# Kernel tuning notes

Hardware: AMD Instinct MI355X
Metric: run time of the kernel (lower is better)

The kernel has to match this reference:

```python
import jax, jax.numpy as jnp
import numpy as np

BATCH, SEQ_LEN, D_MODEL, STATE_DIM = 8, 4096, 512, 64
LN_EPS = 1e-5


def _hippo_log_neg_eigs(state_dim):
    A = np.zeros((state_dim, state_dim))
    for i in range(state_dim):
        for j in range(state_dim):
            if i > j:
                A[i, j] = -((2 * i + 1) ** 0.5) * ((2 * j + 1) ** 0.5)
            elif i == j:
                A[i, j] = -(i + 1)
    ev = np.sort(np.linalg.eigvals(A).real)[:state_dim]
    return np.log(-ev + 1e-06).astype(np.float32)


def setup_inputs() -> dict:
    key = jax.random.key(0)
    ks = jax.random.split(key, 8)
    d, s = D_MODEL, STATE_DIM
    return {
        "x": jax.random.normal(ks[0], (BATCH, SEQ_LEN, d), dtype=jnp.float32),
        "log_A": jnp.asarray(_hippo_log_neg_eigs(s)),
        "B": jax.random.normal(ks[1], (d, s), dtype=jnp.float32) * 0.01,
        "C": jax.random.normal(ks[2], (s, d), dtype=jnp.float32) * 0.01,
        "D": jnp.zeros((d,), dtype=jnp.float32),
        "log_dt": jnp.zeros((), dtype=jnp.float32),
        "gamma": jnp.ones((d,), dtype=jnp.float32),
        "beta": jnp.zeros((d,), dtype=jnp.float32),
        "W1": jax.random.normal(ks[3], (d, 2 * d), dtype=jnp.float32) * (1.0 / np.sqrt(d)),
        "b1": jnp.zeros((2 * d,), dtype=jnp.float32),
        "W2": jax.random.normal(ks[4], (2 * d, d), dtype=jnp.float32) * (1.0 / np.sqrt(2 * d)),
        "b2": jnp.zeros((d,), dtype=jnp.float32),
    }


def _layernorm(x, gamma, beta):
    mu = jnp.mean(x, axis=-1, keepdims=True)
    var = jnp.mean(jnp.square(x - mu), axis=-1, keepdims=True)
    return (x - mu) * jax.lax.rsqrt(var + LN_EPS) * gamma + beta


def reference(x, log_A, B, C, D, log_dt, gamma, beta, W1, b1, W2, b2):
    residual = x
    xn = _layernorm(x, gamma, beta)  # [B, L, D]

    dt = jnp.exp(log_dt)
    A_bar = jnp.exp(-jnp.exp(log_A) * dt)  # [S]

    # Precompute input projections for all timesteps, then scan the diagonal recurrence.
    xB = jnp.einsum("bld,ds->lbs", xn, B)  # [L, B, S]
    h0 = jnp.zeros((xn.shape[0], A_bar.shape[0]), dtype=xn.dtype)

    def step(h, xb_t):
        h = A_bar * h + xb_t
        return h, h

    _, hs = jax.lax.scan(step, h0, xB)  # hs: [L, B, S]

    y = jnp.einsum("lbs,sd->bld", hs, C) + xn * D  # [B, L, D]
    y = y + residual

    yn = _layernorm(y, gamma, beta)
    mlp = jax.nn.gelu(yn @ W1 + b1, approximate=False) @ W2 + b2
    return y + mlp
```

## Files before the change

### kernel.cpp

```cpp
#include <hip/hip_runtime.h>
#include <math.h>

#define BATCH 8
#define SEQL 4096
#define DMODEL 512
#define SDIM 64
#define MROWS (BATCH * SEQL)
#define LN_EPS 1e-5f

typedef __attribute__((ext_vector_type(8))) short bf16x8;
typedef __attribute__((ext_vector_type(4))) float f32x4;

__device__ __forceinline__ float wave_sum(float v) {
#pragma unroll
  for (int off = 32; off > 0; off >>= 1) v += __shfl_xor(v, off, 64);
  return v;
}

__device__ __forceinline__ unsigned short f2bf(float f) {
  unsigned int u = __float_as_uint(f);
  u += 0x7fffu + ((u >> 16) & 1u);
  return (unsigned short)(u >> 16);
}

__device__ __forceinline__ float gelu_exact(float v) {
  return 0.5f * v * (1.0f + erff(v * 0.70710678118654752f));
}

__device__ __forceinline__ void gl2lds16(const void* g, void* l) {
  __builtin_amdgcn_global_load_lds((const __attribute__((address_space(1))) void*)g,
                                   (__attribute__((address_space(3))) void*)l, 16, 0, 0);
}

__global__ void ln_stats_kernel(const float* __restrict__ x, float* __restrict__ mu,
                                float* __restrict__ rstd) {
  int row = blockIdx.x * 4 + (threadIdx.x >> 6);
  int lane = threadIdx.x & 63;
  const float4* xp = (const float4*)(x + (size_t)row * DMODEL);
  float4 a = xp[lane * 2];
  float4 b = xp[lane * 2 + 1];
  float s = a.x + a.y + a.z + a.w + b.x + b.y + b.z + b.w;
  float q = a.x * a.x + a.y * a.y + a.z * a.z + a.w * a.w + b.x * b.x + b.y * b.y +
            b.z * b.z + b.w * b.w;
  s = wave_sum(s);
  q = wave_sum(q);
  if (lane == 0) {
    float m = s * (1.0f / DMODEL);
    float var = q * (1.0f / DMODEL) - m * m;
    mu[row] = m;
    rstd[row] = rsqrtf(var + LN_EPS);
  }
}

__global__ __launch_bounds__(256) void xb_gemm_kernel(
    const float* __restrict__ x, const float* __restrict__ mu, const float* __restrict__ rstd,
    const float* __restrict__ gamma, const float* __restrict__ beta,
    const float* __restrict__ Bm, float* __restrict__ xB) {
  __shared__ float aT[32 * 68];
  __shared__ float bT[32 * 64];
  const int t = threadIdx.x;
  const int m0 = blockIdx.x * 64;
  const int ty = t >> 4, tx = t & 15;
  const int r0 = ty * 4, c0 = tx * 4;
  const int lrow = t >> 2, lseg = t & 3;
  const int bk = t >> 3, bseg = t & 7;
  const float mr = mu[m0 + lrow];
  const float rr = rstd[m0 + lrow];
  float acc[4][4] = {};
  for (int k0 = 0; k0 < DMODEL; k0 += 32) {
    __syncthreads();
    {
      const float* xp = x + (size_t)(m0 + lrow) * DMODEL + k0 + lseg * 8;
      float4 v0 = *(const float4*)xp;
      float4 v1 = *(const float4*)(xp + 4);
      float4 g0 = *(const float4*)(gamma + k0 + lseg * 8);
      float4 g1 = *(const float4*)(gamma + k0 + lseg * 8 + 4);
      float4 e0 = *(const float4*)(beta + k0 + lseg * 8);
      float4 e1 = *(const float4*)(beta + k0 + lseg * 8 + 4);
      const int kb = lseg * 8;
      aT[(kb + 0) * 68 + lrow] = (v0.x - mr) * rr * g0.x + e0.x;
      aT[(kb + 1) * 68 + lrow] = (v0.y - mr) * rr * g0.y + e0.y;
      aT[(kb + 2) * 68 + lrow] = (v0.z - mr) * rr * g0.z + e0.z;
      aT[(kb + 3) * 68 + lrow] = (v0.w - mr) * rr * g0.w + e0.w;
      aT[(kb + 4) * 68 + lrow] = (v1.x - mr) * rr * g1.x + e1.x;
      aT[(kb + 5) * 68 + lrow] = (v1.y - mr) * rr * g1.y + e1.y;
      aT[(kb + 6) * 68 + lrow] = (v1.z - mr) * rr * g1.z + e1.z;
      aT[(kb + 7) * 68 + lrow] = (v1.w - mr) * rr * g1.w + e1.w;
      const float* bp = Bm + (size_t)(k0 + bk) * SDIM + bseg * 8;
      *(float4*)&bT[bk * 64 + bseg * 8] = *(const float4*)bp;
      *(float4*)&bT[bk * 64 + bseg * 8 + 4] = *(const float4*)(bp + 4);
    }
    __syncthreads();
#pragma unroll
    for (int kk = 0; kk < 32; ++kk) {
      float4 av = *(const float4*)&aT[kk * 68 + r0];
      float4 bv = *(const float4*)&bT[kk * 64 + c0];
      float ar[4] = {av.x, av.y, av.z, av.w};
      float br[4] = {bv.x, bv.y, bv.z, bv.w};
#pragma unroll
      for (int i = 0; i < 4; ++i)
#pragma unroll
        for (int j = 0; j < 4; ++j) acc[i][j] += ar[i] * br[j];
    }
  }
#pragma unroll
  for (int i = 0; i < 4; ++i) {
    *(float4*)&xB[(size_t)(m0 + r0 + i) * SDIM + c0] =
        make_float4(acc[i][0], acc[i][1], acc[i][2], acc[i][3]);
  }
}

__global__ void scan_ends_kernel(const float* __restrict__ xB, const float* __restrict__ logA,
                                 const float* __restrict__ logdt, float* __restrict__ ends) {
  int t = blockIdx.x * 256 + threadIdx.x;
  int s = t & 63;
  int c = (t >> 6) & 63;
  int b = t >> 12;
  float a = expf(-expf(logA[s]) * expf(logdt[0]));
  const float* p = xB + ((size_t)(b * SEQL + c * 64)) * SDIM + s;
  float e = 0.0f;
#pragma unroll
  for (int i = 0; i < 64; ++i) e = a * e + p[(size_t)i * SDIM];
  ends[(b * 64 + c) * 64 + s] = e;
}

__global__ void scan_carry_kernel(const float* __restrict__ ends, const float* __restrict__ logA,
                                  const float* __restrict__ logdt,
                                  float* __restrict__ carries) {
  int t = blockIdx.x * 256 + threadIdx.x;
  int s = t & 63;
  int b = t >> 6;
  float a = expf(-expf(logA[s]) * expf(logdt[0]));
  float a64 = a;
#pragma unroll
  for (int i = 0; i < 6; ++i) a64 *= a64;
  float carry = 0.0f;
  for (int c = 0; c < 64; ++c) {
    carries[(b * 64 + c) * 64 + s] = carry;
    carry = a64 * carry + ends[(b * 64 + c) * 64 + s];
  }
}

__global__ void scan_fix_kernel(const float* __restrict__ logA, const float* __restrict__ logdt,
                                const float* __restrict__ carries, float* __restrict__ xB) {
  int t = blockIdx.x * 256 + threadIdx.x;
  int s = t & 63;
  int c = (t >> 6) & 63;
  int b = t >> 12;
  float a = expf(-expf(logA[s]) * expf(logdt[0]));
  float h = carries[(b * 64 + c) * 64 + s];
  float* p = xB + ((size_t)(b * SEQL + c * 64)) * SDIM + s;
#pragma unroll
  for (int i = 0; i < 64; ++i) {
    h = a * h + p[(size_t)i * SDIM];
    p[(size_t)i * SDIM] = h;
  }
}

__global__ __launch_bounds__(256) void y_gemm_kernel(
    const float* __restrict__ hs, const float* __restrict__ Cm, const float* __restrict__ x,
    const float* __restrict__ mu, const float* __restrict__ rstd,
    const float* __restrict__ gamma, const float* __restrict__ beta,
    const float* __restrict__ Dv, float* __restrict__ out) {
  __shared__ float aT[64 * 68];
  __shared__ float bT[64 * 64];
  const int t = threadIdx.x;
  const int m0 = blockIdx.y * 64;
  const int n0 = blockIdx.x * 64;
  const int ty = t >> 4, tx = t & 15;
  const int r0 = ty * 4, c0 = tx * 4;
  const int lrow = t >> 2, lseg = t & 3;
  {
    const float* hp = hs + (size_t)(m0 + lrow) * SDIM + lseg * 16;
#pragma unroll
    for (int u = 0; u < 4; ++u) {
      float4 v = *(const float4*)(hp + u * 4);
      int kb = lseg * 16 + u * 4;
      aT[(kb + 0) * 68 + lrow] = v.x;
      aT[(kb + 1) * 68 + lrow] = v.y;
      aT[(kb + 2) * 68 + lrow] = v.z;
      aT[(kb + 3) * 68 + lrow] = v.w;
    }
    const float* cp = Cm + (size_t)lrow * DMODEL + n0 + lseg * 16;
#pragma unroll
    for (int u = 0; u < 4; ++u)
      *(float4*)&bT[lrow * 64 + lseg * 16 + u * 4] = *(const float4*)(cp + u * 4);
  }
  __syncthreads();
  float acc[4][4] = {};
#pragma unroll 16
  for (int kk = 0; kk < 64; ++kk) {
    float4 av = *(const float4*)&aT[kk * 68 + r0];
    float4 bv = *(const float4*)&bT[kk * 64 + c0];
    float ar[4] = {av.x, av.y, av.z, av.w};
    float br[4] = {bv.x, bv.y, bv.z, bv.w};
#pragma unroll
    for (int i = 0; i < 4; ++i)
#pragma unroll
      for (int j = 0; j < 4; ++j) acc[i][j] += ar[i] * br[j];
  }
  const int cg = n0 + c0;
  float4 gv = *(const float4*)&gamma[cg];
  float4 ev = *(const float4*)&beta[cg];
  float4 dv = *(const float4*)&Dv[cg];
#pragma unroll
  for (int i = 0; i < 4; ++i) {
    int m = m0 + r0 + i;
    float4 xv = *(const float4*)&x[(size_t)m * DMODEL + cg];
    float mm = mu[m], rr = rstd[m];
    float o0 = acc[i][0] + ((xv.x - mm) * rr * gv.x + ev.x) * dv.x + xv.x;
    float o1 = acc[i][1] + ((xv.y - mm) * rr * gv.y + ev.y) * dv.y + xv.y;
    float o2 = acc[i][2] + ((xv.z - mm) * rr * gv.z + ev.z) * dv.z + xv.z;
    float o3 = acc[i][3] + ((xv.w - mm) * rr * gv.w + ev.w) * dv.w + xv.w;
    *(float4*)&out[(size_t)m * DMODEL + cg] = make_float4(o0, o1, o2, o3);
  }
}

__global__ void ln_apply_kernel(const float* __restrict__ y, const float* __restrict__ gamma,
                                const float* __restrict__ beta,
                                unsigned short* __restrict__ yn) {
  int row = blockIdx.x * 4 + (threadIdx.x >> 6);
  int lane = threadIdx.x & 63;
  const float4* yp = (const float4*)(y + (size_t)row * DMODEL);
  float4 a = yp[lane * 2];
  float4 b = yp[lane * 2 + 1];
  float s = a.x + a.y + a.z + a.w + b.x + b.y + b.z + b.w;
  float q = a.x * a.x + a.y * a.y + a.z * a.z + a.w * a.w + b.x * b.x + b.y * b.y +
            b.z * b.z + b.w * b.w;
  s = wave_sum(s);
  q = wave_sum(q);
  float m = s * (1.0f / DMODEL);
  float var = q * (1.0f / DMODEL) - m * m;
  float rs = rsqrtf(var + LN_EPS);
  const float4* gp = (const float4*)gamma;
  const float4* bp = (const float4*)beta;
  float4 g0 = gp[lane * 2], g1 = gp[lane * 2 + 1];
  float4 e0 = bp[lane * 2], e1 = bp[lane * 2 + 1];
  float o0x = (a.x - m) * rs * g0.x + e0.x, o0y = (a.y - m) * rs * g0.y + e0.y;
  float o0z = (a.z - m) * rs * g0.z + e0.z, o0w = (a.w - m) * rs * g0.w + e0.w;
  float o1x = (b.x - m) * rs * g1.x + e1.x, o1y = (b.y - m) * rs * g1.y + e1.y;
  float o1z = (b.z - m) * rs * g1.z + e1.z, o1w = (b.w - m) * rs * g1.w + e1.w;
  uint4 pk;
  pk.x = (unsigned)f2bf(o0x) | ((unsigned)f2bf(o0y) << 16);
  pk.y = (unsigned)f2bf(o0z) | ((unsigned)f2bf(o0w) << 16);
  pk.z = (unsigned)f2bf(o1x) | ((unsigned)f2bf(o1y) << 16);
  pk.w = (unsigned)f2bf(o1z) | ((unsigned)f2bf(o1w) << 16);
  ((uint4*)(yn + (size_t)row * DMODEL))[lane] = pk;
}

__global__ __launch_bounds__(256) void transpose_bf16_kernel(const float* __restrict__ W,
                                                             unsigned short* __restrict__ Wt,
                                                             int K, int N) {
  __shared__ unsigned short tile[64][65];
  int k0 = blockIdx.y * 64, n0 = blockIdx.x * 64;
  int tx = threadIdx.x & 15, ty = threadIdx.x >> 4;
#pragma unroll
  for (int p = 0; p < 4; ++p) {
    int k = p * 16 + ty;
    float4 v = *(const float4*)&W[(size_t)(k0 + k) * N + n0 + tx * 4];
    tile[tx * 4 + 0][k] = f2bf(v.x);
    tile[tx * 4 + 1][k] = f2bf(v.y);
    tile[tx * 4 + 2][k] = f2bf(v.z);
    tile[tx * 4 + 3][k] = f2bf(v.w);
  }
  __syncthreads();
#pragma unroll
  for (int p = 0; p < 4; ++p) {
    int n = p * 16 + ty;
    ushort4 o;
    o.x = tile[n][tx * 4 + 0];
    o.y = tile[n][tx * 4 + 1];
    o.z = tile[n][tx * 4 + 2];
    o.w = tile[n][tx * 4 + 3];
    *(ushort4*)&Wt[(size_t)(n0 + n) * K + k0 + tx * 4] = o;
  }
}

__global__ __launch_bounds__(256) void mlp1_mfma_kernel(const unsigned short* __restrict__ yn,
                                                        const unsigned short* __restrict__ w1t,
                                                        const float* __restrict__ b1,
                                                        unsigned short* __restrict__ g) {
  __shared__ unsigned short As[128 * 32];
  __shared__ unsigned short Bs[128 * 32];
  const int t = threadIdx.x;
  const int wave = t >> 6, lane = t & 63;
  const int m0 = blockIdx.y * 128, n0 = blockIdx.x * 128;
  const int wm = (wave >> 1) * 64, wn = (wave & 1) * 64;
  const int row0 = t >> 2, seg0 = t & 3;
  const int row1 = (t + 256) >> 2, seg1 = t & 3;
  const unsigned short* gA0 = yn + (size_t)(m0 + row0) * 512 + seg0 * 8;
  const unsigned short* gA1 = yn + (size_t)(m0 + row1) * 512 + seg1 * 8;
  const unsigned short* gB0 = w1t + (size_t)(n0 + row0) * 512 + seg0 * 8;
  const unsigned short* gB1 = w1t + (size_t)(n0 + row1) * 512 + seg1 * 8;
  unsigned short* lA0 = As + (size_t)(wave * 64) * 8;
  unsigned short* lA1 = As + (size_t)(256 + wave * 64) * 8;
  unsigned short* lB0 = Bs + (size_t)(wave * 64) * 8;
  unsigned short* lB1 = Bs + (size_t)(256 + wave * 64) * 8;
  f32x4 acc[4][4] = {};
  const int fr = lane & 15, fq = lane >> 4;
  for (int k0 = 0; k0 < 512; k0 += 32) {
    __syncthreads();
    gl2lds16(gA0 + k0, lA0);
    gl2lds16(gA1 + k0, lA1);
    gl2lds16(gB0 + k0, lB0);
    gl2lds16(gB1 + k0, lB1);
    __syncthreads();
#pragma unroll
    for (int i = 0; i < 4; ++i) {
      bf16x8 a = *(const bf16x8*)&As[(wm + i * 16 + fr) * 32 + fq * 8];
#pragma unroll
      for (int j = 0; j < 4; ++j) {
        bf16x8 b = *(const bf16x8*)&Bs[(wn + j * 16 + fr) * 32 + fq * 8];
        acc[i][j] = __builtin_amdgcn_mfma_f32_16x16x32_bf16(a, b, acc[i][j], 0, 0, 0);
      }
    }
  }
#pragma unroll
  for (int i = 0; i < 4; ++i)
#pragma unroll
    for (int j = 0; j < 4; ++j) {
      const int cg = n0 + wn + j * 16 + fr;
      const float bb = b1[cg];
#pragma unroll
      for (int r = 0; r < 4; ++r) {
        const int rg = m0 + wm + i * 16 + fq * 4 + r;
        g[(size_t)rg * 1024 + cg] = f2bf(gelu_exact(acc[i][j][r] + bb));
      }
    }
}

__global__ __launch_bounds__(256) void mlp2_mfma_kernel(const unsigned short* __restrict__ g,
                                                        const unsigned short* __restrict__ w2t,
                                                        const float* __restrict__ b2,
                                                        float* __restrict__ out) {
  __shared__ unsigned short As[128 * 32];
  __shared__ unsigned short Bs[128 * 32];
  const int t = threadIdx.x;
  const int wave = t >> 6, lane = t & 63;
  const int m0 = blockIdx.y * 128, n0 = blockIdx.x * 128;
  const int wm = (wave >> 1) * 64, wn = (wave & 1) * 64;
  const int row0 = t >> 2, seg0 = t & 3;
  const int row1 = (t + 256) >> 2, seg1 = t & 3;
  const unsigned short* gA0 = g + (size_t)(m0 + row0) * 1024 + seg0 * 8;
  const unsigned short* gA1 = g + (size_t)(m0 + row1) * 1024 + seg1 * 8;
  const unsigned short* gB0 = w2t + (size_t)(n0 + row0) * 1024 + seg0 * 8;
  const unsigned short* gB1 = w2t + (size_t)(n0 + row1) * 1024 + seg1 * 8;
  unsigned short* lA0 = As + (size_t)(wave * 64) * 8;
  unsigned short* lA1 = As + (size_t)(256 + wave * 64) * 8;
  unsigned short* lB0 = Bs + (size_t)(wave * 64) * 8;
  unsigned short* lB1 = Bs + (size_t)(256 + wave * 64) * 8;
  f32x4 acc[4][4] = {};
  const int fr = lane & 15, fq = lane >> 4;
  for (int k0 = 0; k0 < 1024; k0 += 32) {
    __syncthreads();
    gl2lds16(gA0 + k0, lA0);
    gl2lds16(gA1 + k0, lA1);
    gl2lds16(gB0 + k0, lB0);
    gl2lds16(gB1 + k0, lB1);
    __syncthreads();
#pragma unroll
    for (int i = 0; i < 4; ++i) {
      bf16x8 a = *(const bf16x8*)&As[(wm + i * 16 + fr) * 32 + fq * 8];
#pragma unroll
      for (int j = 0; j < 4; ++j) {
        bf16x8 b = *(const bf16x8*)&Bs[(wn + j * 16 + fr) * 32 + fq * 8];
        acc[i][j] = __builtin_amdgcn_mfma_f32_16x16x32_bf16(a, b, acc[i][j], 0, 0, 0);
      }
    }
  }
#pragma unroll
  for (int i = 0; i < 4; ++i)
#pragma unroll
    for (int j = 0; j < 4; ++j) {
      const int cg = n0 + wn + j * 16 + fr;
      const float bb = b2[cg];
#pragma unroll
      for (int r = 0; r < 4; ++r) {
        const int rg = m0 + wm + i * 16 + fq * 4 + r;
        const size_t off = (size_t)rg * 512 + cg;
        out[off] = out[off] + acc[i][j][r] + bb;
      }
    }
}

extern "C" void kernel_launch(void* const* d_in, const int* in_sizes, int n_in, void* d_out,
                              int out_size, void* d_ws, size_t ws_size, hipStream_t stream) {
  const float* x = (const float*)d_in[0];
  const float* logA = (const float*)d_in[1];
  const float* Bm = (const float*)d_in[2];
  const float* Cm = (const float*)d_in[3];
  const float* Dv = (const float*)d_in[4];
  const float* logdt = (const float*)d_in[5];
  const float* gamma = (const float*)d_in[6];
  const float* beta = (const float*)d_in[7];
  const float* W1 = (const float*)d_in[8];
  const float* b1 = (const float*)d_in[9];
  const float* W2 = (const float*)d_in[10];
  const float* b2 = (const float*)d_in[11];
  float* out = (float*)d_out;

  char* ws = (char*)d_ws;
  float* mu1 = (float*)(ws + 0);
  float* rstd1 = (float*)(ws + 131072);
  float* ends = (float*)(ws + 262144);
  float* carries = (float*)(ws + 393216);
  float* xB = (float*)(ws + 524288);
  unsigned short* yn = (unsigned short*)(ws + 8912896);
  unsigned short* g = (unsigned short*)(ws + 42467328);
  unsigned short* w1t = (unsigned short*)(ws + 109576192);
  unsigned short* w2t = (unsigned short*)(ws + 110624768);

  transpose_bf16_kernel<<<dim3(1024 / 64, 512 / 64), 256, 0, stream>>>(W1, w1t, 512, 1024);
  transpose_bf16_kernel<<<dim3(512 / 64, 1024 / 64), 256, 0, stream>>>(W2, w2t, 1024, 512);

  ln_stats_kernel<<<MROWS / 4, 256, 0, stream>>>(x, mu1, rstd1);
  xb_gemm_kernel<<<MROWS / 64, 256, 0, stream>>>(x, mu1, rstd1, gamma, beta, Bm, xB);
  scan_ends_kernel<<<128, 256, 0, stream>>>(xB, logA, logdt, ends);
  scan_carry_kernel<<<2, 256, 0, stream>>>(ends, logA, logdt, carries);
  scan_fix_kernel<<<128, 256, 0, stream>>>(logA, logdt, carries, xB);
  y_gemm_kernel<<<dim3(DMODEL / 64, MROWS / 64), 256, 0, stream>>>(xB, Cm, x, mu1, rstd1, gamma,
                                                                   beta, Dv, out);
  ln_apply_kernel<<<MROWS / 4, 256, 0, stream>>>(out, gamma, beta, yn);
  mlp1_mfma_kernel<<<dim3(1024 / 128, MROWS / 128), 256, 0, stream>>>(yn, w1t, b1, g);
  mlp2_mfma_kernel<<<dim3(512 / 128, MROWS / 128), 256, 0, stream>>>(g, w2t, b2, out);
}
```

Baseline: 368.9 us.

## Move SSM projections to bf16 MFMA, fuse y GEMM with second layernorm

The input projection x·B now runs on bf16 MFMA. LayerNorm is folded algebraically: gamma is pre-multiplied into B, and the mean and beta terms are applied in the epilogue from precomputed sums, with x converted to bf16 during the stats pass. The scan writes hidden states as bf16, and one fused kernel computes the C projection with MFMA, the residual, and the second layernorm, producing both out and the bf16 normalized activations. Exact erf GELU is replaced by a polynomial approximation. This removes the fp32 FMA GEMMs and one full pass over the activations, at the cost of extra bf16 rounding and larger LDS use in the fused kernel.

```diff
diff --git a/kernel.cpp b/kernel.cpp
--- a/kernel.cpp
+++ b/kernel.cpp
@@ -23,8 +23,16 @@
   return (unsigned short)(u >> 16);
 }
 
-__device__ __forceinline__ float gelu_exact(float v) {
-  return 0.5f * v * (1.0f + erff(v * 0.70710678118654752f));
+__device__ __forceinline__ float gelu_fast(float v) {
+  float s = v * 0.70710678118654752f;
+  float ax = fabsf(s);
+  float t = 1.0f / (1.0f + 0.3275911f * ax);
+  float p = ((((1.061405429f * t - 1.453152027f) * t + 1.421413741f) * t - 0.284496736f) * t +
+             0.254829592f) *
+            t;
+  float er = 1.0f - p * __expf(-ax * ax);
+  er = copysignf(er, s);
+  return 0.5f * v * (1.0f + er);
 }
 
 __device__ __forceinline__ void gl2lds16(const void* g, void* l) {
@@ -33,7 +41,7 @@
 }
 
 __global__ void ln_stats_kernel(const float* __restrict__ x, float* __restrict__ mu,
-                                float* __restrict__ rstd) {
+                                float* __restrict__ rstd, unsigned short* __restrict__ xbf) {
   int row = blockIdx.x * 4 + (threadIdx.x >> 6);
   int lane = threadIdx.x & 63;
   const float4* xp = (const float4*)(x + (size_t)row * DMODEL);
@@ -44,6 +52,12 @@
             b.z * b.z + b.w * b.w;
   s = wave_sum(s);
   q = wave_sum(q);
+  uint4 pk;
+  pk.x = (unsigned)f2bf(a.x) | ((unsigned)f2bf(a.y) << 16);
+  pk.y = (unsigned)f2bf(a.z) | ((unsigned)f2bf(a.w) << 16);
+  pk.z = (unsigned)f2bf(b.x) | ((unsigned)f2bf(b.y) << 16);
+  pk.w = (unsigned)f2bf(b.z) | ((unsigned)f2bf(b.w) << 16);
+  ((uint4*)(xbf + (size_t)row * DMODEL))[lane] = pk;
   if (lane == 0) {
     float m = s * (1.0f / DMODEL);
     float var = q * (1.0f / DMODEL) - m * m;
@@ -52,62 +66,102 @@
   }
 }
 
-__global__ __launch_bounds__(256) void xb_gemm_kernel(
-    const float* __restrict__ x, const float* __restrict__ mu, const float* __restrict__ rstd,
-    const float* __restrict__ gamma, const float* __restrict__ beta,
-    const float* __restrict__ Bm, float* __restrict__ xB) {
-  __shared__ float aT[32 * 68];
-  __shared__ float bT[32 * 64];
+__global__ void prep_b_kernel(const float* __restrict__ Bm, const float* __restrict__ gamma,
+                              const float* __restrict__ beta, unsigned short* __restrict__ Bgt,
+                              float* __restrict__ gB, float* __restrict__ bB) {
+  int s = blockIdx.x;
+  int l = threadIdx.x;
+  float gs = 0.0f, bs = 0.0f;
+  unsigned short tmp[8];
+#pragma unroll
+  for (int u = 0; u < 8; ++u) {
+    int d = l * 8 + u;
+    float bv = Bm[(size_t)d * SDIM + s];
+    float gv = gamma[d], ev = beta[d];
+    gs += gv * bv;
+    bs += ev * bv;
+    tmp[u] = f2bf(gv * bv);
+  }
+  *(ushort4*)&Bgt[(size_t)s * DMODEL + l * 8] = make_ushort4(tmp[0], tmp[1], tmp[2], tmp[3]);
+  *(ushort4*)&Bgt[(size_t)s * DMODEL + l * 8 + 4] = make_ushort4(tmp[4], tmp[5], tmp[6], tmp[7]);
+  gs = wave_sum(gs);
+  bs = wave_sum(bs);
+  if (l == 0) {
+    gB[s] = gs;
+    bB[s] = bs;
+  }
+}
+
+__global__ __launch_bounds__(256) void transpose_bf16_kernel(const float* __restrict__ W,
+                                                             unsigned short* __restrict__ Wt,
+                                                             int K, int N) {
+  __shared__ unsigned short tile[64][65];
+  int k0 = blockIdx.y * 64, n0 = blockIdx.x * 64;
+  int tx = threadIdx.x & 15, ty = threadIdx.x >> 4;
+#pragma unroll
+  for (int p = 0; p < 4; ++p) {
+    int k = p * 16 + ty;
+    float4 v = *(const float4*)&W[(size_t)(k0 + k) * N + n0 + tx * 4];
+    tile[tx * 4 + 0][k] = f2bf(v.x);
+    tile[tx * 4 + 1][k] = f2bf(v.y);
+    tile[tx * 4 + 2][k] = f2bf(v.z);
+    tile[tx * 4 + 3][k] = f2bf(v.w);
+  }
+  __syncthreads();
+#pragma unroll
+  for (int p = 0; p < 4; ++p) {
+    int n = p * 16 + ty;
+    ushort4 o;
+    o.x = tile[n][tx * 4 + 0];
+    o.y = tile[n][tx * 4 + 1];
+    o.z = tile[n][tx * 4 + 2];
+    o.w = tile[n][tx * 4 + 3];
+    *(ushort4*)&Wt[(size_t)(n0 + n) * K + k0 + tx * 4] = o;
+  }
+}
+
+__global__ __launch_bounds__(256) void xb_mfma_kernel(
+    const unsigned short* __restrict__ xbf, const unsigned short* __restrict__ Bgt,
+    const float* __restrict__ mu, const float* __restrict__ rstd, const float* __restrict__ gB,
+    const float* __restrict__ bB, float* __restrict__ xB) {
+  __shared__ unsigned short As[128 * 32];
+  __shared__ unsigned short Bs[64 * 32];
   const int t = threadIdx.x;
-  const int m0 = blockIdx.x * 64;
-  const int ty = t >> 4, tx = t & 15;
-  const int r0 = ty * 4, c0 = tx * 4;
-  const int lrow = t >> 2, lseg = t & 3;
-  const int bk = t >> 3, bseg = t & 7;
-  const float mr = mu[m0 + lrow];
-  const float rr = rstd[m0 + lrow];
-  float acc[4][4] = {};
+  const int wave = t >> 6, lane = t & 63;
+  const int m0 = blockIdx.x * 128;
+  const int wm = wave * 32;
+  const int row = t >> 2, seg = t & 3;
+  const int fr = lane & 15, fq = lane >> 4;
+  f32x4 acc[2][4] = {};
   for (int k0 = 0; k0 < DMODEL; k0 += 32) {
     __syncthreads();
-    {
-      const float* xp = x + (size_t)(m0 + lrow) * DMODEL + k0 + lseg * 8;
-      float4 v0 = *(const float4*)xp;
-      float4 v1 = *(const float4*)(xp + 4);
-      float4 g0 = *(const float4*)(gamma + k0 + lseg * 8);
-      float4 g1 = *(const float4*)(gamma + k0 + lseg * 8 + 4);
-      float4 e0 = *(const float4*)(beta + k0 + lseg * 8);
-      float4 e1 = *(const float4*)(beta + k0 + lseg * 8 + 4);
-      const int kb = lseg * 8;
-      aT[(kb + 0) * 68 + lrow] = (v0.x - mr) * rr * g0.x + e0.x;
-      aT[(kb + 1) * 68 + lrow] = (v0.y - mr) * rr * g0.y + e0.y;
-      aT[(kb + 2) * 68 + lrow] = (v0.z - mr) * rr * g0.z + e0.z;
-      aT[(kb + 3) * 68 + lrow] = (v0.w - mr) * rr * g0.w + e0.w;
-      aT[(kb + 4) * 68 + lrow] = (v1.x - mr) * rr * g1.x + e1.x;
-      aT[(kb + 5) * 68 + lrow] = (v1.y - mr) * rr * g1.y + e1.y;
-      aT[(kb + 6) * 68 + lrow] = (v1.z - mr) * rr * g1.z + e1.z;
-      aT[(kb + 7) * 68 + lrow] = (v1.w - mr) * rr * g1.w + e1.w;
-      const float* bp = Bm + (size_t)(k0 + bk) * SDIM + bseg * 8;
-      *(float4*)&bT[bk * 64 + bseg * 8] = *(const float4*)bp;
-      *(float4*)&bT[bk * 64 + bseg * 8 + 4] = *(const float4*)(bp + 4);
-    }
-    __syncthreads();
-#pragma unroll
-    for (int kk = 0; kk < 32; ++kk) {
-      float4 av = *(const float4*)&aT[kk * 68 + r0];
-      float4 bv = *(const float4*)&bT[kk * 64 + c0];
-      float ar[4] = {av.x, av.y, av.z, av.w};
-      float br[4] = {bv.x, bv.y, bv.z, bv.w};
-#pragma unroll
-      for (int i = 0; i < 4; ++i)
-#pragma unroll
-        for (int j = 0; j < 4; ++j) acc[i][j] += ar[i] * br[j];
-    }
-  }
-#pragma unroll
-  for (int i = 0; i < 4; ++i) {
-    *(float4*)&xB[(size_t)(m0 + r0 + i) * SDIM + c0] =
-        make_float4(acc[i][0], acc[i][1], acc[i][2], acc[i][3]);
-  }
+    gl2lds16(xbf + (size_t)(m0 + row) * DMODEL + k0 + seg * 8, As + (size_t)(wave * 16) * 32);
+    gl2lds16(xbf + (size_t)(m0 + 64 + row) * DMODEL + k0 + seg * 8,
+             As + (size_t)(64 + wave * 16) * 32);
+    gl2lds16(Bgt + (size_t)row * DMODEL + k0 + seg * 8, Bs + (size_t)(wave * 16) * 32);
+    __syncthreads();
+#pragma unroll
+    for (int i = 0; i < 2; ++i) {
+      bf16x8 a = *(const bf16x8*)&As[(wm + i * 16 + fr) * 32 + fq * 8];
+#pragma unroll
+      for (int j = 0; j < 4; ++j) {
+        bf16x8 b = *(const bf16x8*)&Bs[(j * 16 + fr) * 32 + fq * 8];
+        acc[i][j] = __builtin_amdgcn_mfma_f32_16x16x32_bf16(a, b, acc[i][j], 0, 0, 0);
+      }
+    }
+  }
+#pragma unroll
+  for (int i = 0; i < 2; ++i)
+#pragma unroll
+    for (int r = 0; r < 4; ++r) {
+      const int m = m0 + wm + i * 16 + fq * 4 + r;
+      const float rr = rstd[m], negmurr = -mu[m] * rstd[m];
+#pragma unroll
+      for (int j = 0; j < 4; ++j) {
+        const int s = j * 16 + fr;
+        xB[(size_t)m * SDIM + s] = rr * acc[i][j][r] + negmurr * gB[s] + bB[s];
+      }
+    }
 }
 
 __global__ void scan_ends_kernel(const float* __restrict__ xB, const float* __restrict__ logA,
@@ -142,137 +196,131 @@
 }
 
 __global__ void scan_fix_kernel(const float* __restrict__ logA, const float* __restrict__ logdt,
-                                const float* __restrict__ carries, float* __restrict__ xB) {
+                                const float* __restrict__ carries, const float* __restrict__ xB,
+                                unsigned short* __restrict__ hsb) {
   int t = blockIdx.x * 256 + threadIdx.x;
   int s = t & 63;
   int c = (t >> 6) & 63;
   int b = t >> 12;
   float a = expf(-expf(logA[s]) * expf(logdt[0]));
   float h = carries[(b * 64 + c) * 64 + s];
-  float* p = xB + ((size_t)(b * SEQL + c * 64)) * SDIM + s;
+  const float* p = xB + ((size_t)(b * SEQL + c * 64)) * SDIM + s;
+  unsigned short* q = hsb + ((size_t)(b * SEQL + c * 64)) * SDIM + s;
 #pragma unroll
   for (int i = 0; i < 64; ++i) {
     h = a * h + p[(size_t)i * SDIM];
-    p[(size_t)i * SDIM] = h;
-  }
-}
-
-__global__ __launch_bounds__(256) void y_gemm_kernel(
-    const float* __restrict__ hs, const float* __restrict__ Cm, const float* __restrict__ x,
-    const float* __restrict__ mu, const float* __restrict__ rstd,
+    q[(size_t)i * SDIM] = f2bf(h);
+  }
+}
+
+__global__ __launch_bounds__(256, 2) void y_ln_fused_kernel(
+    const unsigned short* __restrict__ hsb, const unsigned short* __restrict__ ctb,
+    const float* __restrict__ x, const float* __restrict__ mu1, const float* __restrict__ rstd1,
     const float* __restrict__ gamma, const float* __restrict__ beta,
-    const float* __restrict__ Dv, float* __restrict__ out) {
-  __shared__ float aT[64 * 68];
-  __shared__ float bT[64 * 64];
+    const float* __restrict__ Dv, float* __restrict__ out, unsigned short* __restrict__ yn) {
+  __shared__ unsigned short As[64 * 64];
+  __shared__ unsigned short Bs[512 * 64];
+  __shared__ float redS[64 * 4], redQ[64 * 4], meanA[64], rsA[64];
   const int t = threadIdx.x;
-  const int m0 = blockIdx.y * 64;
-  const int n0 = blockIdx.x * 64;
-  const int ty = t >> 4, tx = t & 15;
-  const int r0 = ty * 4, c0 = tx * 4;
-  const int lrow = t >> 2, lseg = t & 3;
+  const int w = t >> 6, lane = t & 63;
+  const int m0 = blockIdx.x * 64;
+  const int fr = lane & 15, fq = lane >> 4;
   {
-    const float* hp = hs + (size_t)(m0 + lrow) * SDIM + lseg * 16;
-#pragma unroll
-    for (int u = 0; u < 4; ++u) {
-      float4 v = *(const float4*)(hp + u * 4);
-      int kb = lseg * 16 + u * 4;
-      aT[(kb + 0) * 68 + lrow] = v.x;
-      aT[(kb + 1) * 68 + lrow] = v.y;
-      aT[(kb + 2) * 68 + lrow] = v.z;
-      aT[(kb + 3) * 68 + lrow] = v.w;
-    }
-    const float* cp = Cm + (size_t)lrow * DMODEL + n0 + lseg * 16;
-#pragma unroll
-    for (int u = 0; u < 4; ++u)
-      *(float4*)&bT[lrow * 64 + lseg * 16 + u * 4] = *(const float4*)(cp + u * 4);
+    const int arow = t >> 3, aseg = t & 7;
+    gl2lds16(hsb + (size_t)(m0 + arow) * SDIM + aseg * 8, As + (size_t)(w * 8) * 64);
+    gl2lds16(hsb + (size_t)(m0 + 32 + arow) * SDIM + aseg * 8,
+             As + (size_t)(32 + w * 8) * 64);
+#pragma unroll
+    for (int c = 0; c < 16; ++c)
+      gl2lds16(ctb + (size_t)c * 2048 + (size_t)t * 8, Bs + (size_t)c * 2048 + (size_t)w * 512);
   }
   __syncthreads();
-  float acc[4][4] = {};
-#pragma unroll 16
-  for (int kk = 0; kk < 64; ++kk) {
-    float4 av = *(const float4*)&aT[kk * 68 + r0];
-    float4 bv = *(const float4*)&bT[kk * 64 + c0];
-    float ar[4] = {av.x, av.y, av.z, av.w};
-    float br[4] = {bv.x, bv.y, bv.z, bv.w};
+  f32x4 acc[4][8] = {};
+#pragma unroll
+  for (int k0 = 0; k0 < 64; k0 += 32) {
+    bf16x8 a[4];
+#pragma unroll
+    for (int i = 0; i < 4; ++i) a[i] = *(const bf16x8*)&As[(i * 16 + fr) * 64 + k0 + fq * 8];
+#pragma unroll
+    for (int j = 0; j < 8; ++j) {
+      bf16x8 b = *(const bf16x8*)&Bs[(w * 128 + j * 16 + fr) * 64 + k0 + fq * 8];
+#pragma unroll
+      for (int i = 0; i < 4; ++i)
+        acc[i][j] = __builtin_amdgcn_mfma_f32_16x16x32_bf16(a[i], b, acc[i][j], 0, 0, 0);
+    }
+  }
+  float sum_[4][4] = {}, sq_[4][4] = {};
+  float mm[4][4], rr[4][4];
+#pragma unroll
+  for (int i = 0; i < 4; ++i)
+#pragma unroll
+    for (int r = 0; r < 4; ++r) {
+      int m = m0 + i * 16 + fq * 4 + r;
+      mm[i][r] = mu1[m];
+      rr[i][r] = rstd1[m];
+    }
+#pragma unroll
+  for (int j = 0; j < 8; ++j) {
+    const int n = w * 128 + j * 16 + fr;
+    const float ga = gamma[n], be = beta[n], dd = Dv[n];
 #pragma unroll
     for (int i = 0; i < 4; ++i)
 #pragma unroll
-      for (int j = 0; j < 4; ++j) acc[i][j] += ar[i] * br[j];
-  }
-  const int cg = n0 + c0;
-  float4 gv = *(const float4*)&gamma[cg];
-  float4 ev = *(const float4*)&beta[cg];
-  float4 dv = *(const float4*)&Dv[cg];
-#pragma unroll
-  for (int i = 0; i < 4; ++i) {
-    int m = m0 + r0 + i;
-    float4 xv = *(const float4*)&x[(size_t)m * DMODEL + cg];
-    float mm = mu[m], rr = rstd[m];
-    float o0 = acc[i][0] + ((xv.x - mm) * rr * gv.x + ev.x) * dv.x + xv.x;
-    float o1 = acc[i][1] + ((xv.y - mm) * rr * gv.y + ev.y) * dv.y + xv.y;
-    float o2 = acc[i][2] + ((xv.z - mm) * rr * gv.z + ev.z) * dv.z + xv.z;
-    float o3 = acc[i][3] + ((xv.w - mm) * rr * gv.w + ev.w) * dv.w + xv.w;
-    *(float4*)&out[(size_t)m * DMODEL + cg] = make_float4(o0, o1, o2, o3);
-  }
-}
-
-__global__ void ln_apply_kernel(const float* __restrict__ y, const float* __restrict__ gamma,
-                                const float* __restrict__ beta,
-                                unsigned short* __restrict__ yn) {
-  int row = blockIdx.x * 4 + (threadIdx.x >> 6);
-  int lane = threadIdx.x & 63;
-  const float4* yp = (const float4*)(y + (size_t)row * DMODEL);
-  float4 a = yp[lane * 2];
-  float4 b = yp[lane * 2 + 1];
-  float s = a.x + a.y + a.z + a.w + b.x + b.y + b.z + b.w;
-  float q = a.x * a.x + a.y * a.y + a.z * a.z + a.w * a.w + b.x * b.x + b.y * b.y +
-            b.z * b.z + b.w * b.w;
-  s = wave_sum(s);
-  q = wave_sum(q);
-  float m = s * (1.0f / DMODEL);
-  float var = q * (1.0f / DMODEL) - m * m;
-  float rs = rsqrtf(var + LN_EPS);
-  const float4* gp = (const float4*)gamma;
-  const float4* bp = (const float4*)beta;
-  float4 g0 = gp[lane * 2], g1 = gp[lane * 2 + 1];
-  float4 e0 = bp[lane * 2], e1 = bp[lane * 2 + 1];
-  float o0x = (a.x - m) * rs * g0.x + e0.x, o0y = (a.y - m) * rs * g0.y + e0.y;
-  float o0z = (a.z - m) * rs * g0.z + e0.z, o0w = (a.w - m) * rs * g0.w + e0.w;
-  float o1x = (b.x - m) * rs * g1.x + e1.x, o1y = (b.y - m) * rs * g1.y + e1.y;
-  float o1z = (b.z - m) * rs * g1.z + e1.z, o1w = (b.w - m) * rs * g1.w + e1.w;
-  uint4 pk;
-  pk.x = (unsigned)f2bf(o0x) | ((unsigned)f2bf(o0y) << 16);
-  pk.y = (unsigned)f2bf(o0z) | ((unsigned)f2bf(o0w) << 16);
-  pk.z = (unsigned)f2bf(o1x) | ((unsigned)f2bf(o1y) << 16);
-  pk.w = (unsigned)f2bf(o1z) | ((unsigned)f2bf(o1w) << 16);
-  ((uint4*)(yn + (size_t)row * DMODEL))[lane] = pk;
-}
-
-__global__ __launch_bounds__(256) void transpose_bf16_kernel(const float* __restrict__ W,
-                                                             unsigned short* __restrict__ Wt,
-                                                             int K, int N) {
-  __shared__ unsigned short tile[64][65];
-  int k0 = blockIdx.y * 64, n0 = blockIdx.x * 64;
-  int tx = threadIdx.x & 15, ty = threadIdx.x >> 4;
-#pragma unroll
-  for (int p = 0; p < 4; ++p) {
-    int k = p * 16 + ty;
-    float4 v = *(const float4*)&W[(size_t)(k0 + k) * N + n0 + tx * 4];
-    tile[tx * 4 + 0][k] = f2bf(v.x);
-    tile[tx * 4 + 1][k] = f2bf(v.y);
-    tile[tx * 4 + 2][k] = f2bf(v.z);
-    tile[tx * 4 + 3][k] = f2bf(v.w);
+      for (int r = 0; r < 4; ++r) {
+        const int m = m0 + i * 16 + fq * 4 + r;
+        const float xv = x[(size_t)m * DMODEL + n];
+        float yv = acc[i][j][r] + ((xv - mm[i][r]) * rr[i][r] * ga + be) * dd + xv;
+        acc[i][j][r] = yv;
+        out[(size_t)m * DMODEL + n] = yv;
+        sum_[i][r] += yv;
+        sq_[i][r] += yv * yv;
+      }
+  }
+#pragma unroll
+  for (int i = 0; i < 4; ++i)
+#pragma unroll
+    for (int r = 0; r < 4; ++r) {
+      float s = sum_[i][r], q = sq_[i][r];
+#pragma unroll
+      for (int off = 1; off < 16; off <<= 1) {
+        s += __shfl_xor(s, off, 64);
+        q += __shfl_xor(q, off, 64);
+      }
+      sum_[i][r] = s;
+      sq_[i][r] = q;
+    }
+  if (fr == 0) {
+#pragma unroll
+    for (int i = 0; i < 4; ++i)
+#pragma unroll
+      for (int r = 0; r < 4; ++r) {
+        const int rl = i * 16 + fq * 4 + r;
+        redS[rl * 4 + w] = sum_[i][r];
+        redQ[rl * 4 + w] = sq_[i][r];
+      }
   }
   __syncthreads();
-#pragma unroll
-  for (int p = 0; p < 4; ++p) {
-    int n = p * 16 + ty;
-    ushort4 o;
-    o.x = tile[n][tx * 4 + 0];
-    o.y = tile[n][tx * 4 + 1];
-    o.z = tile[n][tx * 4 + 2];
-    o.w = tile[n][tx * 4 + 3];
-    *(ushort4*)&Wt[(size_t)(n0 + n) * K + k0 + tx * 4] = o;
+  if (t < 64) {
+    float s = redS[t * 4] + redS[t * 4 + 1] + redS[t * 4 + 2] + redS[t * 4 + 3];
+    float q = redQ[t * 4] + redQ[t * 4 + 1] + redQ[t * 4 + 2] + redQ[t * 4 + 3];
+    float mean = s * (1.0f / DMODEL);
+    float var = q * (1.0f / DMODEL) - mean * mean;
+    meanA[t] = mean;
+    rsA[t] = rsqrtf(var + LN_EPS);
+  }
+  __syncthreads();
+#pragma unroll
+  for (int j = 0; j < 8; ++j) {
+    const int n = w * 128 + j * 16 + fr;
+    const float ga = gamma[n], be = beta[n];
+#pragma unroll
+    for (int i = 0; i < 4; ++i)
+#pragma unroll
+      for (int r = 0; r < 4; ++r) {
+        const int rl = i * 16 + fq * 4 + r;
+        const float yv = acc[i][j][r];
+        yn[(size_t)(m0 + rl) * DMODEL + n] = f2bf((yv - meanA[rl]) * rsA[rl] * ga + be);
+      }
   }
 }
 
@@ -287,11 +335,11 @@
   const int m0 = blockIdx.y * 128, n0 = blockIdx.x * 128;
   const int wm = (wave >> 1) * 64, wn = (wave & 1) * 64;
   const int row0 = t >> 2, seg0 = t & 3;
-  const int row1 = (t + 256) >> 2, seg1 = t & 3;
+  const int row1 = (t + 256) >> 2;
   const unsigned short* gA0 = yn + (size_t)(m0 + row0) * 512 + seg0 * 8;
-  const unsigned short* gA1 = yn + (size_t)(m0 + row1) * 512 + seg1 * 8;
+  const unsigned short* gA1 = yn + (size_t)(m0 + row1) * 512 + seg0 * 8;
   const unsigned short* gB0 = w1t + (size_t)(n0 + row0) * 512 + seg0 * 8;
-  const unsigned short* gB1 = w1t + (size_t)(n0 + row1) * 512 + seg1 * 8;
+  const unsigned short* gB1 = w1t + (size_t)(n0 + row1) * 512 + seg0 * 8;
   unsigned short* lA0 = As + (size_t)(wave * 64) * 8;
   unsigned short* lA1 = As + (size_t)(256 + wave * 64) * 8;
   unsigned short* lB0 = Bs + (size_t)(wave * 64) * 8;
@@ -324,7 +372,7 @@
 #pragma unroll
       for (int r = 0; r < 4; ++r) {
         const int rg = m0 + wm + i * 16 + fq * 4 + r;
-        g[(size_t)rg * 1024 + cg] = f2bf(gelu_exact(acc[i][j][r] + bb));
+        g[(size_t)rg * 1024 + cg] = f2bf(gelu_fast(acc[i][j][r] + bb));
       }
     }
 }
@@ -340,11 +388,11 @@
   const int m0 = blockIdx.y * 128, n0 = blockIdx.x * 128;
   const int wm = (wave >> 1) * 64, wn = (wave & 1) * 64;
   const int row0 = t >> 2, seg0 = t & 3;
-  const int row1 = (t + 256) >> 2, seg1 = t & 3;
+  const int row1 = (t + 256) >> 2;
   const unsigned short* gA0 = g + (size_t)(m0 + row0) * 1024 + seg0 * 8;
-  const unsigned short* gA1 = g + (size_t)(m0 + row1) * 1024 + seg1 * 8;
+  const unsigned short* gA1 = g + (size_t)(m0 + row1) * 1024 + seg0 * 8;
   const unsigned short* gB0 = w2t + (size_t)(n0 + row0) * 1024 + seg0 * 8;
-  const unsigned short* gB1 = w2t + (size_t)(n0 + row1) * 1024 + seg1 * 8;
+  const unsigned short* gB1 = w2t + (size_t)(n0 + row1) * 1024 + seg0 * 8;
   unsigned short* lA0 = As + (size_t)(wave * 64) * 8;
   unsigned short* lA1 = As + (size_t)(256 + wave * 64) * 8;
   unsigned short* lB0 = Bs + (size_t)(wave * 64) * 8;
@@ -404,23 +452,30 @@
   float* rstd1 = (float*)(ws + 131072);
   float* ends = (float*)(ws + 262144);
   float* carries = (float*)(ws + 393216);
-  float* xB = (float*)(ws + 524288);
-  unsigned short* yn = (unsigned short*)(ws + 8912896);
-  unsigned short* g = (unsigned short*)(ws + 42467328);
-  unsigned short* w1t = (unsigned short*)(ws + 109576192);
-  unsigned short* w2t = (unsigned short*)(ws + 110624768);
+  float* gB = (float*)(ws + 524288);
+  float* bB = (float*)(ws + 524800);
+  unsigned short* Bgt = (unsigned short*)(ws + 525312);
+  unsigned short* ctb = (unsigned short*)(ws + 590848);
+  unsigned short* w1t = (unsigned short*)(ws + 656384);
+  unsigned short* w2t = (unsigned short*)(ws + 1704960);
+  unsigned short* g = (unsigned short*)(ws + 2753536);
+  unsigned short* xbf = (unsigned short*)(ws + 2753536);
+  float* xB = (float*)(ws + 69862400);
+  unsigned short* hsb = (unsigned short*)(ws + 78251008);
+  unsigned short* yn = (unsigned short*)(ws + 82445312);
 
   transpose_bf16_kernel<<<dim3(1024 / 64, 512 / 64), 256, 0, stream>>>(W1, w1t, 512, 1024);
   transpose_bf16_kernel<<<dim3(512 / 64, 1024 / 64), 256, 0, stream>>>(W2, w2t, 1024, 512);
-
-  ln_stats_kernel<<<MROWS / 4, 256, 0, stream>>>(x, mu1, rstd1);
-  xb_gemm_kernel<<<MROWS / 64, 256, 0, stream>>>(x, mu1, rstd1, gamma, beta, Bm, xB);
+  transpose_bf16_kernel<<<dim3(512 / 64, 1), 256, 0, stream>>>(Cm, ctb, 64, 512);
+  prep_b_kernel<<<64, 64, 0, stream>>>(Bm, gamma, beta, Bgt, gB, bB);
+
+  ln_stats_kernel<<<MROWS / 4, 256, 0, stream>>>(x, mu1, rstd1, xbf);
+  xb_mfma_kernel<<<MROWS / 128, 256, 0, stream>>>(xbf, Bgt, mu1, rstd1, gB, bB, xB);
   scan_ends_kernel<<<128, 256, 0, stream>>>(xB, logA, logdt, ends);
   scan_carry_kernel<<<2, 256, 0, stream>>>(ends, logA, logdt, carries);
-  scan_fix_kernel<<<128, 256, 0, stream>>>(logA, logdt, carries, xB);
-  y_gemm_kernel<<<dim3(DMODEL / 64, MROWS / 64), 256, 0, stream>>>(xB, Cm, x, mu1, rstd1, gamma,
-                                                                   beta, Dv, out);
-  ln_apply_kernel<<<MROWS / 4, 256, 0, stream>>>(out, gamma, beta, yn);
+  scan_fix_kernel<<<128, 256, 0, stream>>>(logA, logdt, carries, xB, hsb);
+  y_ln_fused_kernel<<<MROWS / 64, 256, 0, stream>>>(hsb, ctb, x, mu1, rstd1, gamma, beta, Dv,
+                                                    out, yn);
   mlp1_mfma_kernel<<<dim3(1024 / 128, MROWS / 128), 256, 0, stream>>>(yn, w1t, b1, g);
   mlp2_mfma_kernel<<<dim3(512 / 128, MROWS / 128), 256, 0, stream>>>(g, w2t, b2, out);
 }
```

Result: slower. 437.1 us (+18.5%).
